# Performance work log

Hardware: AMD Instinct MI355X
Metric: run time of the kernel (lower is better)

## Reference

```python
import jax, jax.numpy as jnp
import numpy as np
from jax import lax

N = 100000      # nodes
F_IN = 128      # dataset.num_features
H = 64          # hidden
E = 1600000     # edges
G = 1000        # graphs (equal-sized, contiguous)
PER = N // G    # nodes per graph = 100
K = 30          # sort-pool k
KS = 3          # conv1d kernel = num_layers


def setup_inputs() -> dict:
    key = jax.random.key(0)
    ks = jax.random.split(key, 20)
    lin = lambda k, i, o: (jax.random.normal(k, (i, o), jnp.float32) / np.sqrt(i)).astype(jnp.float32)
    return {
        "x": jax.random.normal(ks[0], (N, F_IN), jnp.float32),
        "src": jax.random.randint(ks[1], (E,), 0, N, dtype=jnp.int32),
        "dst": jax.random.randint(ks[2], (E,), 0, N, dtype=jnp.int32),
        "num_graphs": G,
        # SAGEConv 1: lin_l (aggr, with bias), lin_r (self, no bias)
        "wl1": lin(ks[3], F_IN, H), "wr1": lin(ks[4], F_IN, H), "b1": jnp.zeros((H,), jnp.float32),
        "wl2": lin(ks[5], H, H), "wr2": lin(ks[6], H, H), "b2": jnp.zeros((H,), jnp.float32),
        "wl3": lin(ks[7], H, H), "wr3": lin(ks[8], H, H), "b3": jnp.zeros((H,), jnp.float32),
        # Conv1d(hidden=64 -> 32, kernel=3): weight [O, I, K]
        "cw": (jax.random.normal(ks[9], (32, H, KS), jnp.float32) / np.sqrt(H * KS)).astype(jnp.float32),
        "cb": jnp.zeros((32,), jnp.float32),
        "w1": lin(ks[10], 32 * (K - KS + 1), H), "bb1": jnp.zeros((H,), jnp.float32),
        "w2": lin(ks[11], H, 1), "bb2": jnp.zeros((1,), jnp.float32),
    }


def _sage(x, src, dst, wl, wr, b, n):
    # PyG SAGEConv (mean aggr): lin_l(mean_{j->i} x_j) + lin_r(x_i)
    msum = jax.ops.segment_sum(x[src], dst, num_segments=n)           # [N, F]
    cnt = jax.ops.segment_sum(jnp.ones((src.shape[0],), x.dtype), dst, num_segments=n)
    mean = msum / jnp.maximum(cnt, 1.0)[:, None]
    return mean @ wl + b + x @ wr


def reference(x, src, dst, num_graphs, wl1, wr1, b1, wl2, wr2, b2, wl3, wr3, b3, cw, cb, w1, bb1, w2, bb2):
    n = x.shape[0]
    h = jax.nn.relu(_sage(x, src, dst, wl1, wr1, b1, n))
    h = jax.nn.relu(_sage(h, src, dst, wl2, wr2, b2, n))
    h = jax.nn.relu(_sage(h, src, dst, wl3, wr3, b3, n))
    # SortAggregation(k): per-graph, sort nodes by last feature channel (desc), keep top-k.
    # batch = contiguous equal-sized graphs -> dense reshape is exact.
    hg = h.reshape(num_graphs, PER, H)                                # [G, PER, H]
    order = jnp.argsort(-hg[:, :, -1], axis=1)[:, :K]                 # [G, K]
    topk = jnp.take_along_axis(hg, order[:, :, None], axis=1)         # [G, K, H]
    xc = jnp.transpose(topk, (0, 2, 1))                               # [G, H, K]
    y = lax.conv_general_dilated(xc, cw, (1,), 'VALID',
                                 dimension_numbers=('NCH', 'OIH', 'NCH'))
    y = jax.nn.relu(y + cb[None, :, None])                            # [G, 32, K-KS+1]
    y = y.reshape(num_graphs, -1)
    y = jax.nn.relu(y @ w1 + bb1)
    # dropout: eval mode -> identity
    return y @ w2 + bb2                                               # [G, 1]
```

## Files before the change

kernel.cpp:

```cpp
#include <hip/hip_runtime.h>

#define NN 100000
#define EE 1600000
#define GG 1000
#define PERG 100
#define KK 30
#define HH 64

#define NB 782
#define CAP 4096
#define CHB 4096
#define BUCKET_BLOCKS ((EE + CHB - 1) / CHB)
#define PROJ_BLOCKS ((NN + 127) / 128)
#define LAYER_BLOCKS ((NN + 63) / 64)

typedef _Float16 half4_t __attribute__((ext_vector_type(4)));
typedef _Float16 half8_t __attribute__((ext_vector_type(8)));

__device__ __forceinline__ void bucket_body(int bid, float* smem,
                                            const int* __restrict__ src,
                                            const int* __restrict__ dst,
                                            int* __restrict__ gcur,
                                            int* __restrict__ pairs) {
  int* lhist = (int*)smem;
  int* lbase = lhist + NB;
  int* lcur = lbase + NB;
  const int t = threadIdx.x;
  const int c0 = bid * CHB;
  const int c1 = min(c0 + CHB, EE);
  for (int b = t; b < NB; b += 256) {
    lhist[b] = 0;
    lcur[b] = 0;
  }
  __syncthreads();
  for (int e = c0 + t; e < c1; e += 256) atomicAdd(&lhist[dst[e] >> 7], 1);
  __syncthreads();
  for (int b = t; b < NB; b += 256) {
    int c = lhist[b];
    lbase[b] = c ? atomicAdd(&gcur[b], c) : 0;
  }
  __syncthreads();
  for (int e = c0 + t; e < c1; e += 256) {
    int d = dst[e];
    int b = d >> 7;
    int p = atomicAdd(&lcur[b], 1);
    pairs[b * CAP + lbase[b] + p] = (src[e] << 7) | (d & 127);
  }
}

template <int K>
__device__ __forceinline__ void proj_body(int bid, float* smem,
                                          const float* __restrict__ X,
                                          const float* __restrict__ WL,
                                          const float* __restrict__ WR,
                                          float* __restrict__ P,
                                          float* __restrict__ R) {
  constexpr int BM = 128, BK = 32, XSP = 36, WSP = 144;
  float* xs = smem;
  float* ws = smem + BM * XSP;
  const int t = threadIdx.x;
  const int row0 = bid * BM;
  const int tc = t & 15, tr = t >> 4;
  const int wcol = tc * 8 + (tc >> 2) * 4;

  float acc[8][8];
#pragma unroll
  for (int i = 0; i < 8; ++i)
#pragma unroll
    for (int j = 0; j < 8; ++j) acc[i][j] = 0.f;

  for (int k0 = 0; k0 < K; k0 += BK) {
    __syncthreads();
    for (int idx = t; idx < BM * 8; idx += 256) {
      int r = idx >> 3, c = idx & 7;
      int row = row0 + r;
      float4 v = make_float4(0.f, 0.f, 0.f, 0.f);
      if (row < NN) v = *reinterpret_cast<const float4*>(&X[(size_t)row * K + k0 + c * 4]);
      *reinterpret_cast<float4*>(&xs[r * XSP + c * 4]) = v;
    }
    for (int idx = t; idx < BK * 16; idx += 256) {
      int kr = idx >> 4, c4 = idx & 15;
      int gcl = c4 >> 1;
      int off = gcl * 8 + (gcl >> 2) * 4 + (c4 & 1) * 4;
      *reinterpret_cast<float4*>(&ws[kr * WSP + off]) =
          *reinterpret_cast<const float4*>(&WL[(k0 + kr) * 64 + c4 * 4]);
      int g2 = gcl + 8;
      int off2 = g2 * 8 + (g2 >> 2) * 4 + (c4 & 1) * 4;
      *reinterpret_cast<float4*>(&ws[kr * WSP + off2]) =
          *reinterpret_cast<const float4*>(&WR[(k0 + kr) * 64 + c4 * 4]);
    }
    __syncthreads();
    for (int kk4 = 0; kk4 < BK; kk4 += 4) {
      float4 a[8];
#pragma unroll
      for (int i = 0; i < 8; ++i)
        a[i] = *reinterpret_cast<const float4*>(&xs[(tr + 16 * i) * XSP + kk4]);
#pragma unroll
      for (int kk = 0; kk < 4; ++kk) {
        float4 b0 = *reinterpret_cast<const float4*>(&ws[(kk4 + kk) * WSP + wcol]);
        float4 b1 = *reinterpret_cast<const float4*>(&ws[(kk4 + kk) * WSP + wcol + 4]);
        float bv[8] = {b0.x, b0.y, b0.z, b0.w, b1.x, b1.y, b1.z, b1.w};
#pragma unroll
        for (int i = 0; i < 8; ++i) {
          float av = (kk == 0) ? a[i].x : (kk == 1) ? a[i].y : (kk == 2) ? a[i].z : a[i].w;
#pragma unroll
          for (int j = 0; j < 8; ++j) acc[i][j] = fmaf(av, bv[j], acc[i][j]);
        }
      }
    }
  }

  float* OUT = (tc < 8) ? P : R;
  int cb = (tc & 7) * 8;
#pragma unroll
  for (int i = 0; i < 8; ++i) {
    int row = row0 + tr + 16 * i;
    if (row < NN) {
      *reinterpret_cast<float4*>(&OUT[(size_t)row * 64 + cb]) =
          make_float4(acc[i][0], acc[i][1], acc[i][2], acc[i][3]);
      *reinterpret_cast<float4*>(&OUT[(size_t)row * 64 + cb + 4]) =
          make_float4(acc[i][4], acc[i][5], acc[i][6], acc[i][7]);
    }
  }
}

__global__ __launch_bounds__(256) void fused_bucket_proj(const int* __restrict__ src,
                                                         const int* __restrict__ dst,
                                                         int* __restrict__ gcur,
                                                         int* __restrict__ pairs,
                                                         const float* __restrict__ X,
                                                         const float* __restrict__ WL,
                                                         const float* __restrict__ WR,
                                                         float* __restrict__ P,
                                                         float* __restrict__ R) {
  __shared__ float smem[128 * 36 + 32 * 144];
  if (blockIdx.x < PROJ_BLOCKS)
    proj_body<128>(blockIdx.x, smem, X, WL, WR, P, R);
  else
    bucket_body(blockIdx.x - PROJ_BLOCKS, smem, src, dst, gcur, pairs);
}

__global__ __launch_bounds__(256) void csr_kernel(const int* __restrict__ gcur,
                                                  const int* __restrict__ pairs,
                                                  int* __restrict__ row_start,
                                                  int* __restrict__ cnt,
                                                  int* __restrict__ eidx) {
  __shared__ int vals[CAP];
  __shared__ int hist[128];
  __shared__ int offs[128];
  __shared__ int cur[128];
  __shared__ int red[4];
  const int b = blockIdx.x;
  const int t = threadIdx.x;
  int s = 0;
  for (int i = t; i < b; i += 256) s += gcur[i];
#pragma unroll
  for (int off = 32; off > 0; off >>= 1) s += __shfl_xor(s, off);
  if ((t & 63) == 0) red[t >> 6] = s;
  if (t < 128) {
    hist[t] = 0;
    cur[t] = 0;
  }
  __syncthreads();
  const int base = red[0] + red[1] + red[2] + red[3];
  const int nb = gcur[b];
  for (int i = t; i < nb; i += 256) {
    int v = pairs[b * CAP + i];
    vals[i] = v;
    atomicAdd(&hist[v & 127], 1);
  }
  __syncthreads();
  if (t < 128) {
    int ss = 0;
    for (int m = 0; m < t; ++m) ss += hist[m];
    offs[t] = ss;
    int node = b * 128 + t;
    if (node < NN) {
      row_start[node] = base + ss;
      cnt[node] = hist[t];
    }
  }
  __syncthreads();
  for (int i = t; i < nb; i += 256) {
    int v = vals[i];
    int ld = v & 127;
    int p = atomicAdd(&cur[ld], 1);
    eidx[base + offs[ld] + p] = v >> 7;
  }
}

template <bool HOUT>
__global__ __launch_bounds__(256) void layer_kernel(const float* __restrict__ P,
                                                    const float* __restrict__ R,
                                                    const float* __restrict__ bias,
                                                    const int* __restrict__ row_start,
                                                    const int* __restrict__ cnt,
                                                    const int* __restrict__ eidx,
                                                    const float* __restrict__ WL,
                                                    const float* __restrict__ WR,
                                                    float* __restrict__ Pout,
                                                    _Float16* __restrict__ PoutH,
                                                    float* __restrict__ Rout,
                                                    float* __restrict__ keyP,
                                                    float* __restrict__ keyR) {
  __shared__ float hs[64 * 68];
  const int t = threadIdx.x;
  const int lane = t & 63;
  const int qd = t >> 4;
  const int ql = t & 15;
  const int row0 = blockIdx.x * 64;

  for (int p = 0; p < 4; ++p) {
    const int r = qd + 16 * p;
    const int node = row0 + r;
    float4 acc = make_float4(0.f, 0.f, 0.f, 0.f);
    if (node < NN) {
      const int base = row_start[node];
      const int deg = cnt[node];
      for (int e0 = 0; e0 < deg; e0 += 16) {
        const int rem = deg - e0;
        const int ii = (ql < rem) ? ql : (rem - 1);
        int idx = eidx[base + e0 + ii];
#pragma unroll
        for (int j = 0; j < 16; ++j) {
          const int sj = __shfl(idx, (lane & 48) | j);
          const float wj = (j < rem) ? 1.f : 0.f;
          const float4 vj = *reinterpret_cast<const float4*>(&P[(size_t)sj * 64 + ql * 4]);
          acc.x = fmaf(wj, vj.x, acc.x);
          acc.y = fmaf(wj, vj.y, acc.y);
          acc.z = fmaf(wj, vj.z, acc.z);
          acc.w = fmaf(wj, vj.w, acc.w);
        }
      }
      const float dv = fmaxf((float)deg, 1.0f);
      const float4 r4 = *reinterpret_cast<const float4*>(&R[(size_t)node * 64 + ql * 4]);
      const float4 b4 = *reinterpret_cast<const float4*>(&bias[ql * 4]);
      acc.x = fmaxf(acc.x / dv + b4.x + r4.x, 0.f);
      acc.y = fmaxf(acc.y / dv + b4.y + r4.y, 0.f);
      acc.z = fmaxf(acc.z / dv + b4.z + r4.z, 0.f);
      acc.w = fmaxf(acc.w / dv + b4.w + r4.w, 0.f);
    }
    *reinterpret_cast<float4*>(&hs[r * 68 + ql * 4]) = acc;
  }
  __syncthreads();

  const int tc = t & 15, tr = t >> 4;
  const float* WB = (tc < 8) ? WL : WR;
  const int wcolg = (tc & 7) * 8;

  float acc[4][8];
#pragma unroll
  for (int i = 0; i < 4; ++i)
#pragma unroll
    for (int j = 0; j < 8; ++j) acc[i][j] = 0.f;

  for (int kk4 = 0; kk4 < 64; kk4 += 4) {
    float4 a[4];
#pragma unroll
    for (int i = 0; i < 4; ++i)
      a[i] = *reinterpret_cast<const float4*>(&hs[(tr + 16 * i) * 68 + kk4]);
#pragma unroll
    for (int kk = 0; kk < 4; ++kk) {
      float4 b0 = *reinterpret_cast<const float4*>(&WB[(kk4 + kk) * 64 + wcolg]);
      float4 b1 = *reinterpret_cast<const float4*>(&WB[(kk4 + kk) * 64 + wcolg + 4]);
      float bv[8] = {b0.x, b0.y, b0.z, b0.w, b1.x, b1.y, b1.z, b1.w};
#pragma unroll
      for (int i = 0; i < 4; ++i) {
        float av = (kk == 0) ? a[i].x : (kk == 1) ? a[i].y : (kk == 2) ? a[i].z : a[i].w;
#pragma unroll
        for (int j = 0; j < 8; ++j) acc[i][j] = fmaf(av, bv[j], acc[i][j]);
      }
    }
  }

  const int cb = (tc & 7) * 8;
  if (tc < 8) {
#pragma unroll
    for (int i = 0; i < 4; ++i) {
      int row = row0 + tr + 16 * i;
      if (row < NN) {
        if (HOUT) {
          half8_t hv;
#pragma unroll
          for (int j = 0; j < 8; ++j) hv[j] = (_Float16)acc[i][j];
          *reinterpret_cast<half8_t*>(&PoutH[(size_t)row * 64 + cb]) = hv;
          if (keyP != nullptr && tc == 7) keyP[row] = acc[i][7];
        } else {
          *reinterpret_cast<float4*>(&Pout[(size_t)row * 64 + cb]) =
              make_float4(acc[i][0], acc[i][1], acc[i][2], acc[i][3]);
          *reinterpret_cast<float4*>(&Pout[(size_t)row * 64 + cb + 4]) =
              make_float4(acc[i][4], acc[i][5], acc[i][6], acc[i][7]);
        }
      }
    }
  } else {
#pragma unroll
    for (int i = 0; i < 4; ++i) {
      int row = row0 + tr + 16 * i;
      if (row < NN) {
        *reinterpret_cast<float4*>(&Rout[(size_t)row * 64 + cb]) =
            make_float4(acc[i][0], acc[i][1], acc[i][2], acc[i][3]);
        *reinterpret_cast<float4*>(&Rout[(size_t)row * 64 + cb + 4]) =
            make_float4(acc[i][4], acc[i][5], acc[i][6], acc[i][7]);
        if (HOUT && keyR != nullptr && tc == 15) keyR[row] = acc[i][7];
      }
    }
  }
}

__global__ __launch_bounds__(256) void sel_head(const _Float16* __restrict__ Ph,
                                                const float* __restrict__ R,
                                                const float* __restrict__ b3,
                                                const float* __restrict__ keyP,
                                                const float* __restrict__ keyR,
                                                const int* __restrict__ row_start,
                                                const int* __restrict__ cnt,
                                                const int* __restrict__ eidx,
                                                const float* __restrict__ cw,
                                                const float* __restrict__ cb,
                                                const float* __restrict__ w1,
                                                const float* __restrict__ bb1,
                                                const float* __restrict__ w2,
                                                const float* __restrict__ bb2,
                                                float* __restrict__ out) {
  __shared__ float key[PERG];
  __shared__ int sel[32];
  __shared__ float feat[34 * 65];
  __shared__ float cwT[192 * 33];
  __shared__ float z[896];
  __shared__ float psum[256];
  const int g = blockIdx.x;
  const int t = threadIdx.x;

  for (int idx = t; idx < 32 * 192; idx += 256) {
    int o = idx / 192, k = idx % 192;
    cwT[k * 33 + o] = cw[idx];
  }
  if (t < PERG) {
    const int node = g * PERG + t;
    const int base = row_start[node];
    const int deg = cnt[node];
    float s = 0.f;
    for (int e = 0; e < deg; ++e) s += keyP[eidx[base + e]];
    key[t] = fmaxf(s / fmaxf((float)deg, 1.f) + b3[63] + keyR[node], 0.f);
  }
  __syncthreads();

  if (t < PERG) {
    float kv = key[t];
    int r = 0;
    for (int m = 0; m < PERG; ++m) {
      float km = key[m];
      r += (int)((km > kv) || (km == kv && m < t));
    }
    if (r < KK) sel[r] = t;
  }
  __syncthreads();

  const int lane = t & 63;
  const int qd = t >> 4;
  const int ql = t & 15;
  for (int p = 0; p < 2; ++p) {
    const int r = qd + 16 * p;
    if (r < KK) {
      const int node = g * PERG + sel[r];
      const int base = row_start[node];
      const int deg = cnt[node];
      float4 acc = make_float4(0.f, 0.f, 0.f, 0.f);
      for (int e0 = 0; e0 < deg; e0 += 16) {
        const int rem = deg - e0;
        const int ii = (ql < rem) ? ql : (rem - 1);
        int idx = eidx[base + e0 + ii];
#pragma unroll
        for (int j = 0; j < 16; ++j) {
          const int sj = __shfl(idx, (lane & 48) | j);
          const float wj = (j < rem) ? 1.f : 0.f;
          const half4_t hv =
              *reinterpret_cast<const half4_t*>(&Ph[(size_t)sj * 64 + ql * 4]);
          acc.x = fmaf(wj, (float)hv.x, acc.x);
          acc.y = fmaf(wj, (float)hv.y, acc.y);
          acc.z = fmaf(wj, (float)hv.z, acc.z);
          acc.w = fmaf(wj, (float)hv.w, acc.w);
        }
      }
      const float dv = fmaxf((float)deg, 1.0f);
      const float4 r4 = *reinterpret_cast<const float4*>(&R[(size_t)node * 64 + ql * 4]);
      const float4 b4 = *reinterpret_cast<const float4*>(&b3[ql * 4]);
      feat[r * 65 + ql * 4 + 0] = fmaxf(acc.x / dv + b4.x + r4.x, 0.f);
      feat[r * 65 + ql * 4 + 1] = fmaxf(acc.y / dv + b4.y + r4.y, 0.f);
      feat[r * 65 + ql * 4 + 2] = fmaxf(acc.z / dv + b4.z + r4.z, 0.f);
      feat[r * 65 + ql * 4 + 3] = fmaxf(acc.w / dv + b4.w + r4.w, 0.f);
    }
  }
  __syncthreads();

  {
    const int o = t & 31;
    const int pg = t >> 5;
    float zacc[4] = {0.f, 0.f, 0.f, 0.f};
    int i = 0, tt = 0;
    for (int k = 0; k < 192; ++k) {
      float c = cwT[k * 33 + o];
#pragma unroll
      for (int j = 0; j < 4; ++j) {
        int p = pg + 8 * j;
        zacc[j] = fmaf(c, feat[(p + tt) * 65 + i], zacc[j]);
      }
      if (++tt == 3) {
        tt = 0;
        ++i;
      }
    }
    float cbo = cb[o];
#pragma unroll
    for (int j = 0; j < 4; ++j) {
      int p = pg + 8 * j;
      if (p < 28) z[o * 28 + p] = fmaxf(zacc[j] + cbo, 0.f);
    }
  }
  __syncthreads();

  {
    const int hh = t & 63;
    const int quarter = t >> 6;
    const int q0 = quarter * 224;
    float acc = 0.f;
    for (int q = 0; q < 224; ++q)
      acc = fmaf(z[q0 + q], w1[(size_t)(q0 + q) * 64 + hh], acc);
    psum[t] = acc;
  }
  __syncthreads();

  if (t < 64) {
    float o1 = fmaxf(bb1[t] + psum[t] + psum[t + 64] + psum[t + 128] + psum[t + 192], 0.f);
    float v = o1 * w2[t];
#pragma unroll
    for (int off = 32; off > 0; off >>= 1) v += __shfl_down(v, off);
    if (t == 0) out[g] = v + bb2[0];
  }
}

extern "C" void kernel_launch(void* const* d_in, const int* in_sizes, int n_in,
                              void* d_out, int out_size, void* d_ws, size_t ws_size,
                              hipStream_t stream) {
  const float* x = (const float*)d_in[0];
  const int* src = (const int*)d_in[1];
  const int* dst = (const int*)d_in[2];
  const float* wl1 = (const float*)d_in[4];
  const float* wr1 = (const float*)d_in[5];
  const float* b1 = (const float*)d_in[6];
  const float* wl2 = (const float*)d_in[7];
  const float* wr2 = (const float*)d_in[8];
  const float* b2 = (const float*)d_in[9];
  const float* wl3 = (const float*)d_in[10];
  const float* wr3 = (const float*)d_in[11];
  const float* b3 = (const float*)d_in[12];
  const float* cw = (const float*)d_in[13];
  const float* cb = (const float*)d_in[14];
  const float* w1 = (const float*)d_in[15];
  const float* bb1 = (const float*)d_in[16];
  const float* w2 = (const float*)d_in[17];
  const float* bb2 = (const float*)d_in[18];
  float* out = (float*)d_out;

  char* w = (char*)d_ws;
  auto carve = [&](size_t bytes) {
    char* p = w;
    w += (bytes + 255) & ~(size_t)255;
    return p;
  };
  int* row_start = (int*)carve((size_t)NN * 4);
  int* cnt = (int*)carve((size_t)NN * 4);
  int* eidx = (int*)carve((size_t)EE * 4);
  float* P1 = (float*)carve((size_t)NN * 64 * 4);
  float* R1 = (float*)carve((size_t)NN * 64 * 4);
  float* P2 = (float*)carve((size_t)NN * 64 * 4);
  float* R2 = (float*)carve((size_t)NN * 64 * 4);
  _Float16* PhF = (_Float16*)carve((size_t)NN * 64 * 2);
  float* keyP = (float*)carve((size_t)NN * 4);
  float* keyR = (float*)carve((size_t)NN * 4);
  int* gcur = (int*)carve((size_t)NB * 4);
  int* pairs = (int*)P2;

  hipMemsetAsync(gcur, 0, (size_t)NB * 4, stream);
  fused_bucket_proj<<<BUCKET_BLOCKS + PROJ_BLOCKS, 256, 0, stream>>>(
      src, dst, gcur, pairs, x, wl1, wr1, P1, R1);
  csr_kernel<<<NB, 256, 0, stream>>>(gcur, pairs, row_start, cnt, eidx);

  layer_kernel<false><<<LAYER_BLOCKS, 256, 0, stream>>>(
      P1, R1, b1, row_start, cnt, eidx, wl2, wr2, P2, nullptr, R2, nullptr, nullptr);
  layer_kernel<true><<<LAYER_BLOCKS, 256, 0, stream>>>(
      P2, R2, b2, row_start, cnt, eidx, wl3, wr3, nullptr, PhF, R1, keyP, keyR);
  sel_head<<<GG, 256, 0, stream>>>(PhF, R1, b3, keyP, keyR, row_start, cnt, eidx,
                                   cw, cb, w1, bb1, w2, bb2, out);
}
```

Before: 436.9 us.

## Shrink projection tile to 64 rows and read weights directly from global

The first-layer projection in the fused bucket/projection kernel now uses 64-row tiles with 4x8 accumulators per thread instead of 128-row tiles with 8x8. The weight tile is no longer staged in shared memory; each thread reads WL/WR rows straight from global (cached) memory. Shared memory per block drops from about 35 KB to under 10 KB and register pressure falls, which should raise occupancy for both the projection and bucketing blocks sharing this kernel. The cost is more global/L1 weight traffic and twice as many projection blocks.

```diff
diff --git a/kernel.cpp b/kernel.cpp
--- a/kernel.cpp
+++ b/kernel.cpp
@@ -11,7 +11,7 @@
 #define CAP 4096
 #define CHB 4096
 #define BUCKET_BLOCKS ((EE + CHB - 1) / CHB)
-#define PROJ_BLOCKS ((NN + 127) / 128)
+#define PROJ64_BLOCKS ((NN + 63) / 64)
 #define LAYER_BLOCKS ((NN + 63) / 64)
 
 typedef _Float16 half4_t __attribute__((ext_vector_type(4)));
@@ -49,59 +49,47 @@
 }
 
 template <int K>
-__device__ __forceinline__ void proj_body(int bid, float* smem,
+__device__ __forceinline__ void proj_body(int bid, float* xs,
                                           const float* __restrict__ X,
                                           const float* __restrict__ WL,
                                           const float* __restrict__ WR,
                                           float* __restrict__ P,
                                           float* __restrict__ R) {
-  constexpr int BM = 128, BK = 32, XSP = 36, WSP = 144;
-  float* xs = smem;
-  float* ws = smem + BM * XSP;
+  constexpr int XSP = 36;
   const int t = threadIdx.x;
-  const int row0 = bid * BM;
+  const int row0 = bid * 64;
   const int tc = t & 15, tr = t >> 4;
-  const int wcol = tc * 8 + (tc >> 2) * 4;
-
-  float acc[8][8];
-#pragma unroll
-  for (int i = 0; i < 8; ++i)
+  const float* WB = (tc < 8) ? WL : WR;
+  const int wcolg = (tc & 7) * 8;
+
+  float acc[4][8];
+#pragma unroll
+  for (int i = 0; i < 4; ++i)
 #pragma unroll
     for (int j = 0; j < 8; ++j) acc[i][j] = 0.f;
 
-  for (int k0 = 0; k0 < K; k0 += BK) {
+  for (int k0 = 0; k0 < K; k0 += 32) {
     __syncthreads();
-    for (int idx = t; idx < BM * 8; idx += 256) {
+    for (int idx = t; idx < 64 * 8; idx += 256) {
       int r = idx >> 3, c = idx & 7;
       int row = row0 + r;
       float4 v = make_float4(0.f, 0.f, 0.f, 0.f);
       if (row < NN) v = *reinterpret_cast<const float4*>(&X[(size_t)row * K + k0 + c * 4]);
       *reinterpret_cast<float4*>(&xs[r * XSP + c * 4]) = v;
     }
-    for (int idx = t; idx < BK * 16; idx += 256) {
-      int kr = idx >> 4, c4 = idx & 15;
-      int gcl = c4 >> 1;
-      int off = gcl * 8 + (gcl >> 2) * 4 + (c4 & 1) * 4;
-      *reinterpret_cast<float4*>(&ws[kr * WSP + off]) =
-          *reinterpret_cast<const float4*>(&WL[(k0 + kr) * 64 + c4 * 4]);
-      int g2 = gcl + 8;
-      int off2 = g2 * 8 + (g2 >> 2) * 4 + (c4 & 1) * 4;
-      *reinterpret_cast<float4*>(&ws[kr * WSP + off2]) =
-          *reinterpret_cast<const float4*>(&WR[(k0 + kr) * 64 + c4 * 4]);
-    }
     __syncthreads();
-    for (int kk4 = 0; kk4 < BK; kk4 += 4) {
-      float4 a[8];
-#pragma unroll
-      for (int i = 0; i < 8; ++i)
+    for (int kk4 = 0; kk4 < 32; kk4 += 4) {
+      float4 a[4];
+#pragma unroll
+      for (int i = 0; i < 4; ++i)
         a[i] = *reinterpret_cast<const float4*>(&xs[(tr + 16 * i) * XSP + kk4]);
 #pragma unroll
       for (int kk = 0; kk < 4; ++kk) {
-        float4 b0 = *reinterpret_cast<const float4*>(&ws[(kk4 + kk) * WSP + wcol]);
-        float4 b1 = *reinterpret_cast<const float4*>(&ws[(kk4 + kk) * WSP + wcol + 4]);
+        float4 b0 = *reinterpret_cast<const float4*>(&WB[(size_t)(k0 + kk4 + kk) * 64 + wcolg]);
+        float4 b1 = *reinterpret_cast<const float4*>(&WB[(size_t)(k0 + kk4 + kk) * 64 + wcolg + 4]);
         float bv[8] = {b0.x, b0.y, b0.z, b0.w, b1.x, b1.y, b1.z, b1.w};
 #pragma unroll
-        for (int i = 0; i < 8; ++i) {
+        for (int i = 0; i < 4; ++i) {
           float av = (kk == 0) ? a[i].x : (kk == 1) ? a[i].y : (kk == 2) ? a[i].z : a[i].w;
 #pragma unroll
           for (int j = 0; j < 8; ++j) acc[i][j] = fmaf(av, bv[j], acc[i][j]);
@@ -111,9 +99,9 @@
   }
 
   float* OUT = (tc < 8) ? P : R;
-  int cb = (tc & 7) * 8;
-#pragma unroll
-  for (int i = 0; i < 8; ++i) {
+  const int cb = (tc & 7) * 8;
+#pragma unroll
+  for (int i = 0; i < 4; ++i) {
     int row = row0 + tr + 16 * i;
     if (row < NN) {
       *reinterpret_cast<float4*>(&OUT[(size_t)row * 64 + cb]) =
@@ -133,11 +121,11 @@
                                                          const float* __restrict__ WR,
                                                          float* __restrict__ P,
                                                          float* __restrict__ R) {
-  __shared__ float smem[128 * 36 + 32 * 144];
-  if (blockIdx.x < PROJ_BLOCKS)
+  __shared__ float smem[2400];
+  if (blockIdx.x < PROJ64_BLOCKS)
     proj_body<128>(blockIdx.x, smem, X, WL, WR, P, R);
   else
-    bucket_body(blockIdx.x - PROJ_BLOCKS, smem, src, dst, gcur, pairs);
+    bucket_body(blockIdx.x - PROJ64_BLOCKS, smem, src, dst, gcur, pairs);
 }
 
 __global__ __launch_bounds__(256) void csr_kernel(const int* __restrict__ gcur,
@@ -483,7 +471,7 @@
   int* pairs = (int*)P2;
 
   hipMemsetAsync(gcur, 0, (size_t)NB * 4, stream);
-  fused_bucket_proj<<<BUCKET_BLOCKS + PROJ_BLOCKS, 256, 0, stream>>>(
+  fused_bucket_proj<<<BUCKET_BLOCKS + PROJ64_BLOCKS, 256, 0, stream>>>(
       src, dst, gcur, pairs, x, wl1, wr1, P1, R1);
   csr_kernel<<<NB, 256, 0, stream>>>(gcur, pairs, row_start, cnt, eidx);
 
```

After: 458.8 us. +5.0%, slower.
